# Optimization experiments

Measured on AMD Instinct MI355X. Metric: run time of the kernel, lower is better.

Reference implementation:

```python
import jax, jax.numpy as jnp
import numpy as np

B = 1024
N_ATOMS = 51
FLAT = 7 * 7 * 64  # conv output: 84->20->9->7 spatial, 64 channels


def _conv(x, w, b, s):
    # x: NCHW, w: OIHW, VALID padding, stride s
    y = jax.lax.conv_general_dilated(
        x, w, window_strides=(s, s), padding='VALID',
        dimension_numbers=('NCHW', 'OIHW', 'NCHW'))
    return y + b[None, :, None, None]


def setup_inputs() -> dict:
    key = jax.random.key(0)
    ks = jax.random.split(key, 8)

    def w(k, shape, fan_in):
        return jax.random.normal(k, shape, dtype=jnp.float32) / np.float32(np.sqrt(fan_in))

    return {
        'x': jax.random.uniform(ks[0], (B, 4, 84, 84), jnp.float32, 0.0, 256.0),
        'cw1': w(ks[1], (32, 4, 8, 8), 4 * 8 * 8), 'cb1': jnp.zeros((32,), jnp.float32),
        'cw2': w(ks[2], (64, 32, 4, 4), 32 * 4 * 4), 'cb2': jnp.zeros((64,), jnp.float32),
        'cw3': w(ks[3], (64, 64, 3, 3), 64 * 3 * 3), 'cb3': jnp.zeros((64,), jnp.float32),
        'fw1': w(ks[4], (FLAT, 256), FLAT), 'fb1': jnp.zeros((256,), jnp.float32),
        'fw2': w(ks[5], (256, N_ATOMS), 256), 'fb2': jnp.zeros((N_ATOMS,), jnp.float32),
        'z': jnp.linspace(-10.0, 10.0, N_ATOMS).astype(jnp.float32),  # support atoms
        'n_out': 6,
    }


def reference(x, cw1, cb1, cw2, cb2, cw3, cb3, fw1, fb1, fw2, fb2, z, n_out):
    x = x / 256.0
    x = jax.nn.relu(_conv(x, cw1, cb1, 4))  # [B,32,20,20]
    x = jax.nn.relu(_conv(x, cw2, cb2, 2))  # [B,64,9,9]
    x = jax.nn.relu(_conv(x, cw3, cb3, 1))  # [B,64,7,7]
    h = x.reshape(x.shape[0], -1)           # [B,3136]
    h = jax.nn.relu(h @ fw1 + fb1)          # [B,256]
    p = jax.nn.softmax(h @ fw2 + fb2, axis=1)  # [B,n_atoms]
    # Original loop writes fc_layers(x)[i] identically for every action j:
    dist = jnp.broadcast_to(p[:, None, :], (p.shape[0], n_out, p.shape[1]))
    res = jnp.einsum('bna,a->bn', dist, z)  # expected value per action
    return (dist, res)
```

## Files before the change

kernel.cpp:

```cpp
#include <hip/hip_runtime.h>
#include <hip/hip_fp16.h>

#define RL(x) __builtin_amdgcn_readfirstlane(x)

typedef _Float16 f16x8 __attribute__((ext_vector_type(8)));
typedef float    f32x16 __attribute__((ext_vector_type(16)));

__global__ __launch_bounds__(256) void wprep_k(const float* __restrict__ w1,
                                               const float* __restrict__ w2,
                                               const float* __restrict__ w3,
                                               float* __restrict__ wt1,
                                               __half* __restrict__ w2h,
                                               float* __restrict__ wt3) {
  int i = blockIdx.x * 256 + threadIdx.x;
  if (i < 8192) {
    int kx = i & 7, j = (i >> 3) & 7, g = (i >> 6) & 3;
    int ky = (i >> 8) & 7, ic = i >> 11;
    wt1[i] = w1[(g * 8 + j) * 256 + ic * 64 + ky * 8 + kx];
  }
  if (i < 32768) {
    int j = i & 7, ln = (i >> 3) & 31, kh = (i >> 8) & 1, ot = (i >> 9) & 1, ic = i >> 10;
    int k = kh * 8 + j, kx = k >> 2, ky = k & 3, oc = ot * 32 + ln;
    w2h[i] = __float2half(w2[oc * 512 + ic * 16 + ky * 4 + kx]);
  }
  if (i < 36864) {
    int o3 = i % 24, o = o3 / 3, kx = o3 - o * 3;
    int r = i / 24, ocg = r & 7, r2 = r >> 3, ky = r2 % 3, ic = r2 / 3;
    wt3[i] = w3[(ocg * 8 + o) * 576 + ic * 9 + ky * 3 + kx];
  }
}

__global__ __launch_bounds__(256, 4) void conv1_k(const float* __restrict__ x,
                                                  const float* __restrict__ wt,
                                                  const float* __restrict__ bias,
                                                  __half* __restrict__ out) {
  __shared__ float plane[7056];
  const int b    = blockIdx.x;
  const int tid  = threadIdx.x;
  const int lane = tid & 63;
  const int g    = RL(tid >> 6);

  int pv[7], ib[7];
#pragma unroll
  for (int s = 0; s < 7; ++s) {
    int p = lane + 64 * s;
    pv[s] = (p < 400);
    if (p > 399) p = 399;
    int py = p / 20, px = p - py * 20;
    ib[s] = py * 336 + px * 4;
  }

  float acc[7][8];
#pragma unroll
  for (int s = 0; s < 7; ++s)
#pragma unroll
    for (int j = 0; j < 8; ++j) acc[s][j] = 0.f;

  const float* xb = x + b * 28224;

#pragma unroll 1
  for (int ici = 0; ici < 4; ++ici) {
    const int ic = (ici + (b >> 8)) & 3;
    if (ici) __syncthreads();
    const float* xp = xb + ic * 7056;
#pragma unroll
    for (int i = 0; i < 7; ++i) {
      int idx = tid + i * 256;
      if (idx < 1764) {
        float4 v = *(const float4*)(xp + idx * 4);
        *(float4*)&plane[idx * 4] = v;
      }
    }
    __syncthreads();

#pragma unroll 1
    for (int ky = 0; ky < 8; ++ky) {
      const float* wp = wt + (ic * 8 + ky) * 256 + g * 64;
      float wr[8][8];
#pragma unroll
      for (int j = 0; j < 8; ++j) {
        float4 w0 = *(const float4*)(wp + j * 8);
        float4 w1 = *(const float4*)(wp + j * 8 + 4);
        wr[j][0]=w0.x; wr[j][1]=w0.y; wr[j][2]=w0.z; wr[j][3]=w0.w;
        wr[j][4]=w1.x; wr[j][5]=w1.y; wr[j][6]=w1.z; wr[j][7]=w1.w;
      }
      const float* rp = plane + ky * 84;
#pragma unroll
      for (int s = 0; s < 7; ++s) {
        float4 a = *(const float4*)(rp + ib[s]);
        float4 c = *(const float4*)(rp + ib[s] + 4);
        float in8[8] = {a.x, a.y, a.z, a.w, c.x, c.y, c.z, c.w};
#pragma unroll
        for (int j = 0; j < 8; ++j)
#pragma unroll
          for (int kx = 0; kx < 8; ++kx)
            acc[s][j] = fmaf(in8[kx], wr[j][kx], acc[s][j]);
      }
    }
  }

  const float inv256 = 1.0f / 256.0f;
#pragma unroll
  for (int j = 0; j < 8; ++j) {
    float bj = bias[g * 8 + j];
    __half* op = out + (b * 32 + g * 8 + j) * 400;
#pragma unroll
    for (int s = 0; s < 7; ++s) {
      if (pv[s]) {
        float v = acc[s][j] * inv256 + bj;
        op[lane + 64 * s] = __float2half(v > 0.f ? v : 0.f);
      }
    }
  }
}

__global__ __launch_bounds__(256) void t1_k(const __half* __restrict__ in,
                                            __half* __restrict__ out) {
  __shared__ __half t[64][65];
  const int kb = blockIdx.x * 64;
  const int bb = blockIdx.y * 64;
  const int lane = threadIdx.x & 63;
  const int ty   = threadIdx.x >> 6;
#pragma unroll
  for (int r = ty; r < 64; r += 4)
    t[r][lane] = in[(bb + r) * 12800 + kb + lane];
  __syncthreads();
#pragma unroll
  for (int r = ty; r < 64; r += 4)
    out[(kb + r) * 1024 + bb + lane] = t[lane][r];
}

__global__ __launch_bounds__(256, 1) void conv2_k(const __half* __restrict__ in,
                                                  const __half* __restrict__ w2h,
                                                  const float* __restrict__ bias,
                                                  __half* __restrict__ out) {
  __shared__ __align__(16) __half sh[2][9216];
  const int bid = blockIdx.x;
  const int opy = bid % 9;
  const int bt  = bid / 9;
  const int bbase = bt * 64;
  const int tid  = threadIdx.x;
  const int lane = tid & 63;
  const int wv   = RL(tid >> 6);
  const int octile = wv & 1;
  const int bsub   = wv >> 1;
  const int kh = lane >> 5;
  const int ln = lane & 31;

  const unsigned short* inu = (const unsigned short*)in;
  const unsigned short* wu  = (const unsigned short*)w2h;

  int roff[5], offA[5];
#pragma unroll
  for (int p = 0; p < 5; ++p) {
    int idx = p * 256 + tid;
    int px = idx >> 6, b = idx & 63;
    roff[p] = px * 1024 + b;
    offA[p] = b * 128 + ((((px >> 1) ^ (b & 7)) << 3) | ((px & 1) << 2));
  }
  const int base0 = (40 * opy) * 1024 + bbase;

  f32x16 acc[9];
#pragma unroll
  for (int ox = 0; ox < 9; ++ox)
#pragma unroll
    for (int r = 0; r < 16; ++r) acc[ox][r] = 0.f;

  ushort4 s0, s1, s2, s3, s4; uint2 sW;

#define C2_LOAD(icv) do {                                                     \
    const unsigned short* ibp = inu + (icv) * 409600 + base0;                 \
    s0 = make_ushort4(ibp[roff[0]], ibp[roff[0]+20480], ibp[roff[0]+40960], ibp[roff[0]+61440]); \
    s1 = make_ushort4(ibp[roff[1]], ibp[roff[1]+20480], ibp[roff[1]+40960], ibp[roff[1]+61440]); \
    s2 = make_ushort4(ibp[roff[2]], ibp[roff[2]+20480], ibp[roff[2]+40960], ibp[roff[2]+61440]); \
    s3 = make_ushort4(ibp[roff[3]], ibp[roff[3]+20480], ibp[roff[3]+40960], ibp[roff[3]+61440]); \
    s4 = make_ushort4(ibp[roff[4]], ibp[roff[4]+20480], ibp[roff[4]+40960], ibp[roff[4]+61440]); \
    sW = *(const uint2*)(wu + (icv) * 1024 + tid * 4);                        \
  } while (0)

#define C2_STORE(buf) do {                                                    \
    *(uint2*)&sh[buf][offA[0]] = make_uint2((unsigned)s0.x | ((unsigned)s0.y << 16), (unsigned)s0.z | ((unsigned)s0.w << 16)); \
    *(uint2*)&sh[buf][offA[1]] = make_uint2((unsigned)s1.x | ((unsigned)s1.y << 16), (unsigned)s1.z | ((unsigned)s1.w << 16)); \
    *(uint2*)&sh[buf][offA[2]] = make_uint2((unsigned)s2.x | ((unsigned)s2.y << 16), (unsigned)s2.z | ((unsigned)s2.w << 16)); \
    *(uint2*)&sh[buf][offA[3]] = make_uint2((unsigned)s3.x | ((unsigned)s3.y << 16), (unsigned)s3.z | ((unsigned)s3.w << 16)); \
    *(uint2*)&sh[buf][offA[4]] = make_uint2((unsigned)s4.x | ((unsigned)s4.y << 16), (unsigned)s4.z | ((unsigned)s4.w << 16)); \
    *(uint2*)&sh[buf][8192 + tid * 4] = sW;                                   \
  } while (0)

  const int offW = 8192 + octile * 512 + kh * 256 + ln * 8;
  const int bloc = bsub * 32 + ln;
  const int bx7  = bloc & 7;
  const int brow = bloc * 128;

  int cur = 0;
  C2_LOAD(0);
#pragma unroll 1
  for (int ic = 0; ic < 32; ++ic) {
    __syncthreads();
    C2_STORE(cur);
    const int icn = ic < 31 ? ic + 1 : 31;
    C2_LOAD(icn);
    __syncthreads();
    f16x8 aw = *(const f16x8*)&sh[cur][offW];
#pragma unroll
    for (int ox = 0; ox < 9; ++ox) {
      f16x8 bx = *(const f16x8*)&sh[cur][brow + (((ox + kh) ^ bx7) << 3)];
      acc[ox] = __builtin_amdgcn_mfma_f32_32x32x16_f16(aw, bx, acc[ox], 0, 0, 0);
    }
    cur ^= 1;
  }
#undef C2_LOAD
#undef C2_STORE

  float bv[16];
#pragma unroll
  for (int r = 0; r < 16; ++r)
    bv[r] = bias[octile * 32 + (r & 3) + 8 * (r >> 2) + 4 * kh];
  const int bout = bbase + bloc;
#pragma unroll
  for (int ox = 0; ox < 9; ++ox) {
#pragma unroll
    for (int r = 0; r < 16; ++r) {
      const int oc = octile * 32 + (r & 3) + 8 * (r >> 2) + 4 * kh;
      float v = acc[ox][r] + bv[r];
      out[(oc * 81 + opy * 9 + ox) * 1024 + bout] = __float2half(v > 0.f ? v : 0.f);
    }
  }
}

__global__ __launch_bounds__(128, 2) void conv3_k(const __half* __restrict__ in,
                                                  const float* __restrict__ wt,
                                                  const float* __restrict__ bias,
                                                  __half* __restrict__ out) {
  const int bid = blockIdx.x;
  const int ocg = (bid >> 3) & 15;
  const int grp = ((bid >> 7) << 3) | (bid & 7);
  const int opy = grp % 7;
  const int bg  = grp / 7;
  const int tid  = threadIdx.x;
  const int lane = tid & 63;
  const int wv   = RL(tid >> 6);

  float acc[4][7];
#pragma unroll
  for (int o = 0; o < 4; ++o)
#pragma unroll
    for (int ox = 0; ox < 7; ++ox) acc[o][ox] = 0.f;

  const __half* ib = in + bg * 64 + lane;
  const int ic0 = wv * 32;

#pragma unroll 1
  for (int ici = 0; ici < 32; ++ici) {
    const int ic = ic0 + ici;
#pragma unroll
    for (int ky = 0; ky < 3; ++ky) {
      const float* wp = wt + ((ic * 3 + ky) * 8 + (ocg >> 1)) * 24 + (ocg & 1) * 12;
      float wk[12];
#pragma unroll
      for (int q = 0; q < 12; ++q) wk[q] = wp[q];
      const __half* rp = ib + (ic * 81 + (opy + ky) * 9) * 1024;
      float iv[9];
#pragma unroll
      for (int q = 0; q < 9; ++q) iv[q] = __half2float(rp[q * 1024]);
#pragma unroll
      for (int o = 0; o < 4; ++o)
#pragma unroll
        for (int ox = 0; ox < 7; ++ox)
#pragma unroll
          for (int kx = 0; kx < 3; ++kx)
            acc[o][ox] = fmaf(iv[ox + kx], wk[o * 3 + kx], acc[o][ox]);
    }
  }

  __shared__ float red[4][7][64];
  if (wv == 1) {
#pragma unroll
    for (int o = 0; o < 4; ++o)
#pragma unroll
      for (int ox = 0; ox < 7; ++ox) red[o][ox][lane] = acc[o][ox];
  }
  __syncthreads();
  if (wv == 0) {
#pragma unroll
    for (int o = 0; o < 4; ++o) {
      const int oc = ocg * 4 + o;
      const float bj = bias[oc];
#pragma unroll
      for (int ox = 0; ox < 7; ++ox) {
        float v = acc[o][ox] + red[o][ox][lane] + bj;
        out[(oc * 49 + opy * 7 + ox) * 1024 + bg * 64 + lane] =
            __float2half(v > 0.f ? v : 0.f);
      }
    }
  }
}

__global__ __launch_bounds__(64, 2) void fc1a_k(const __half* __restrict__ a,
                                                const float* __restrict__ w,
                                                float* __restrict__ part) {
  const int bid = blockIdx.x;
  const int jg  = (bid >> 3) & 15;
  const int grp = ((bid >> 7) << 3) | (bid & 7);
  const int kc  = grp & 15;
  const int bg  = grp >> 4;
  const int lane = threadIdx.x;

  float acc[16];
#pragma unroll
  for (int j = 0; j < 16; ++j) acc[j] = 0.f;

  const __half* ap = a + kc * 196 * 1024 + bg * 64 + lane;
  const float* wp0 = w + kc * 196 * 256 + jg * 16;

#pragma unroll 4
  for (int k = 0; k < 196; ++k) {
    float av = __half2float(ap[k * 1024]);
    const float* wp = wp0 + k * 256;
#pragma unroll
    for (int j = 0; j < 16; ++j) acc[j] = fmaf(av, wp[j], acc[j]);
  }
#pragma unroll
  for (int j = 0; j < 16; ++j)
    part[(kc * 256 + jg * 16 + j) * 1024 + bg * 64 + lane] = acc[j];
}

__global__ __launch_bounds__(256) void fc1b_k(const float* __restrict__ part,
                                              const float* __restrict__ bias,
                                              float* __restrict__ h) {
  int idx = blockIdx.x * 256 + threadIdx.x;
  float s = bias[idx >> 10];
#pragma unroll
  for (int c = 0; c < 16; ++c) s += part[c * 262144 + idx];
  h[idx] = s > 0.f ? s : 0.f;
}

__global__ __launch_bounds__(256) void fc2_k(const float* __restrict__ h,
                                             const float* __restrict__ w,
                                             const float* __restrict__ bias,
                                             const float* __restrict__ z,
                                             float* __restrict__ dist,
                                             float* __restrict__ res) {
  __shared__ float wl[256 * 51];
  const int tid = threadIdx.x;
#pragma unroll
  for (int i = tid; i < 256 * 51; i += 256) wl[i] = w[i];
  __syncthreads();

  const int j   = tid & 63;
  const int b   = blockIdx.x * 4 + RL(tid >> 6);
  const int jc = j < 51 ? j : 50;
  float acc = bias[jc];
#pragma unroll 8
  for (int k = 0; k < 256; ++k)
    acc = fmaf(h[k * 1024 + b], wl[k * 51 + jc], acc);
  float logit = (j < 51) ? acc : -1e30f;
  float m = logit;
#pragma unroll
  for (int o = 32; o > 0; o >>= 1) m = fmaxf(m, __shfl_xor(m, o, 64));
  float e = (j < 51) ? __expf(logit - m) : 0.f;
  float ssum = e;
#pragma unroll
  for (int o = 32; o > 0; o >>= 1) ssum += __shfl_xor(ssum, o, 64);
  float p = e / ssum;
  float zv = (j < 51) ? z[jc] : 0.f;
  float rz = p * zv;
#pragma unroll
  for (int o = 32; o > 0; o >>= 1) rz += __shfl_xor(rz, o, 64);
  if (j < 51) {
    float* db = dist + b * 6 * 51 + j;
#pragma unroll
    for (int n = 0; n < 6; ++n) db[n * 51] = p;
  }
  if (j < 6) res[b * 6 + j] = rz;
}

extern "C" void kernel_launch(void* const* d_in, const int* in_sizes, int n_in,
                              void* d_out, int out_size, void* d_ws, size_t ws_size,
                              hipStream_t stream) {
  const float* x   = (const float*)d_in[0];
  const float* cw1 = (const float*)d_in[1];
  const float* cb1 = (const float*)d_in[2];
  const float* cw2 = (const float*)d_in[3];
  const float* cb2 = (const float*)d_in[4];
  const float* cw3 = (const float*)d_in[5];
  const float* cb3 = (const float*)d_in[6];
  const float* fw1 = (const float*)d_in[7];
  const float* fb1 = (const float*)d_in[8];
  const float* fw2 = (const float*)d_in[9];
  const float* fb2 = (const float*)d_in[10];
  const float* z   = (const float*)d_in[11];

  float* ws = (float*)d_ws;
  __half* c1h = (__half*)ws;
  __half* c1t = (__half*)(ws + 6553600);
  __half* c2t = (__half*)(ws + 13107200);
  __half* c3t = (__half*)(ws + 15761408);
  float*  pw  = ws;
  float*  h_t = ws + 4194304;

  float*  wt3n = (float*)d_out;
  float*  wt1n = (float*)d_out + 36864;
  __half* w2h  = (__half*)((float*)d_out + 45056);

  float* dist = (float*)d_out;
  float* res  = dist + 1024 * 6 * 51;

  wprep_k<<<144, 256, 0, stream>>>(cw1, cw2, cw3, wt1n, w2h, wt3n);
  conv1_k<<<1024, 256, 0, stream>>>(x, wt1n, cb1, c1h);
  t1_k<<<dim3(200, 16), 256, 0, stream>>>(c1h, c1t);
  conv2_k<<<144, 256, 0, stream>>>(c1t, w2h, cb2, c2t);
  conv3_k<<<1792, 128, 0, stream>>>(c2t, wt3n, cb3, c3t);
  fc1a_k<<<4096, 64, 0, stream>>>(c3t, fw1, pw);
  fc1b_k<<<1024, 256, 0, stream>>>(pw, fb1, h_t);
  fc2_k<<<256, 256, 0, stream>>>(h_t, fw2, fb2, z, dist, res);
}
```

Before: 418.5 us.

## Rewrite conv1 as fp16 MFMA implicit GEMM writing transposed output directly

conv1 is rewritten from scalar fp32 FMAs to 32x32x16 fp16 MFMA instructions. Each block stages a 32-image row band of the input into shared memory as fp16, with the 1/256 scaling folded in. Outputs are written straight in the [oc,p,batch] layout that conv2 expects, so the separate transpose kernel and its round trip through global memory are removed. This trades fp32 accuracy for fp16 inputs and gives up some occupancy (launch bounds drop to 2 blocks) in exchange for matrix-core throughput.

```diff
diff --git a/kernel.cpp b/kernel.cpp
--- a/kernel.cpp
+++ b/kernel.cpp
@@ -4,19 +4,19 @@
 #define RL(x) __builtin_amdgcn_readfirstlane(x)
 
 typedef _Float16 f16x8 __attribute__((ext_vector_type(8)));
+typedef _Float16 f16x4 __attribute__((ext_vector_type(4)));
 typedef float    f32x16 __attribute__((ext_vector_type(16)));
 
 __global__ __launch_bounds__(256) void wprep_k(const float* __restrict__ w1,
                                                const float* __restrict__ w2,
                                                const float* __restrict__ w3,
-                                               float* __restrict__ wt1,
+                                               __half* __restrict__ w1h,
                                                __half* __restrict__ w2h,
                                                float* __restrict__ wt3) {
   int i = blockIdx.x * 256 + threadIdx.x;
   if (i < 8192) {
-    int kx = i & 7, j = (i >> 3) & 7, g = (i >> 6) & 3;
-    int ky = (i >> 8) & 7, ic = i >> 11;
-    wt1[i] = w1[(g * 8 + j) * 256 + ic * 64 + ky * 8 + kx];
+    int kx = i & 7, oc = (i >> 3) & 31, ky = (i >> 8) & 7, ic = i >> 11;
+    w1h[i] = __float2half(w1[oc * 256 + ic * 64 + ky * 8 + kx]);
   }
   if (i < 32768) {
     int j = i & 7, ln = (i >> 3) & 31, kh = (i >> 8) & 1, ot = (i >> 9) & 1, ic = i >> 10;
@@ -30,104 +30,85 @@
   }
 }
 
-__global__ __launch_bounds__(256, 4) void conv1_k(const float* __restrict__ x,
-                                                  const float* __restrict__ wt,
+__global__ __launch_bounds__(256, 2) void conv1_k(const float* __restrict__ x,
+                                                  const __half* __restrict__ w1h,
                                                   const float* __restrict__ bias,
                                                   __half* __restrict__ out) {
-  __shared__ float plane[7056];
-  const int b    = blockIdx.x;
-  const int tid  = threadIdx.x;
+  __shared__ __align__(16) __half xs[32256];
+  const int bid = blockIdx.x;
+  const int q  = bid % 10;
+  const int bt = bid / 10;
+  const int tid = threadIdx.x;
   const int lane = tid & 63;
-  const int g    = RL(tid >> 6);
-
-  int pv[7], ib[7];
-#pragma unroll
-  for (int s = 0; s < 7; ++s) {
-    int p = lane + 64 * s;
-    pv[s] = (p < 400);
-    if (p > 399) p = 399;
-    int py = p / 20, px = p - py * 20;
-    ib[s] = py * 336 + px * 4;
-  }
-
-  float acc[7][8];
-#pragma unroll
-  for (int s = 0; s < 7; ++s)
-#pragma unroll
-    for (int j = 0; j < 8; ++j) acc[s][j] = 0.f;
-
-  const float* xb = x + b * 28224;
+  const int wv   = RL(tid >> 6);
+  const int pyl = wv >> 1;
+  const int pxq = wv & 1;
+  const int kh = lane >> 5;
+  const int ln = lane & 31;
+
+  f32x16 acc[10];
+#pragma unroll
+  for (int px = 0; px < 10; ++px)
+#pragma unroll
+    for (int r = 0; r < 16; ++r) acc[px][r] = 0.f;
+
+  const float inv = 1.0f / 256.0f;
+  const float* xb = x + bt * 32 * 28224 + q * 8 * 84;
 
 #pragma unroll 1
-  for (int ici = 0; ici < 4; ++ici) {
-    const int ic = (ici + (b >> 8)) & 3;
-    if (ici) __syncthreads();
-    const float* xp = xb + ic * 7056;
-#pragma unroll
-    for (int i = 0; i < 7; ++i) {
-      int idx = tid + i * 256;
-      if (idx < 1764) {
-        float4 v = *(const float4*)(xp + idx * 4);
-        *(float4*)&plane[idx * 4] = v;
+  for (int ic = 0; ic < 4; ++ic) {
+    if (ic) __syncthreads();
+#pragma unroll 4
+    for (int pass = 0; pass < 32; ++pass) {
+      int item = pass * 256 + tid;
+      if (item < 8064) {
+        int cg = item % 21;
+        int rb = item / 21;
+        int b = rb & 31, r = rb >> 5;
+        const float* gp = xb + b * 28224 + ic * 7056 + r * 84 + cg * 4;
+        float4 v = *(const float4*)gp;
+        __half2 h01 = __floats2half2_rn(v.x * inv, v.y * inv);
+        __half2 h23 = __floats2half2_rn(v.z * inv, v.w * inv);
+        *(uint2*)&xs[(r * 32 + b) * 84 + cg * 4] =
+            make_uint2(*(unsigned*)&h01, *(unsigned*)&h23);
       }
     }
     __syncthreads();
 
-#pragma unroll 1
-    for (int ky = 0; ky < 8; ++ky) {
-      const float* wp = wt + (ic * 8 + ky) * 256 + g * 64;
-      float wr[8][8];
-#pragma unroll
-      for (int j = 0; j < 8; ++j) {
-        float4 w0 = *(const float4*)(wp + j * 8);
-        float4 w1 = *(const float4*)(wp + j * 8 + 4);
-        wr[j][0]=w0.x; wr[j][1]=w0.y; wr[j][2]=w0.z; wr[j][3]=w0.w;
-        wr[j][4]=w1.x; wr[j][5]=w1.y; wr[j][6]=w1.z; wr[j][7]=w1.w;
+#pragma unroll
+    for (int t = 0; t < 4; ++t) {
+      f16x8 aw = *(const f16x8*)(w1h + ((ic * 8 + 2 * t + kh) * 32 + ln) * 8);
+      const __half* rp = &xs[((pyl * 4 + 2 * t + kh) * 32 + ln) * 84];
+#pragma unroll
+      for (int px = 0; px < 10; ++px) {
+        const int xg = pxq * 10 + px;
+        f16x4 lo = *(const f16x4*)(rp + 4 * xg);
+        f16x4 hi = *(const f16x4*)(rp + 4 * xg + 4);
+        f16x8 bx;
+        bx[0]=lo[0]; bx[1]=lo[1]; bx[2]=lo[2]; bx[3]=lo[3];
+        bx[4]=hi[0]; bx[5]=hi[1]; bx[6]=hi[2]; bx[7]=hi[3];
+        acc[px] = __builtin_amdgcn_mfma_f32_32x32x16_f16(aw, bx, acc[px], 0, 0, 0);
       }
-      const float* rp = plane + ky * 84;
-#pragma unroll
-      for (int s = 0; s < 7; ++s) {
-        float4 a = *(const float4*)(rp + ib[s]);
-        float4 c = *(const float4*)(rp + ib[s] + 4);
-        float in8[8] = {a.x, a.y, a.z, a.w, c.x, c.y, c.z, c.w};
-#pragma unroll
-        for (int j = 0; j < 8; ++j)
-#pragma unroll
-          for (int kx = 0; kx < 8; ++kx)
-            acc[s][j] = fmaf(in8[kx], wr[j][kx], acc[s][j]);
-      }
-    }
-  }
-
-  const float inv256 = 1.0f / 256.0f;
-#pragma unroll
-  for (int j = 0; j < 8; ++j) {
-    float bj = bias[g * 8 + j];
-    __half* op = out + (b * 32 + g * 8 + j) * 400;
-#pragma unroll
-    for (int s = 0; s < 7; ++s) {
-      if (pv[s]) {
-        float v = acc[s][j] * inv256 + bj;
-        op[lane + 64 * s] = __float2half(v > 0.f ? v : 0.f);
-      }
-    }
-  }
-}
-
-__global__ __launch_bounds__(256) void t1_k(const __half* __restrict__ in,
-                                            __half* __restrict__ out) {
-  __shared__ __half t[64][65];
-  const int kb = blockIdx.x * 64;
-  const int bb = blockIdx.y * 64;
-  const int lane = threadIdx.x & 63;
-  const int ty   = threadIdx.x >> 6;
-#pragma unroll
-  for (int r = ty; r < 64; r += 4)
-    t[r][lane] = in[(bb + r) * 12800 + kb + lane];
-  __syncthreads();
-#pragma unroll
-  for (int r = ty; r < 64; r += 4)
-    out[(kb + r) * 1024 + bb + lane] = t[lane][r];
+    }
+  }
+
+  float bv[16];
+#pragma unroll
+  for (int r = 0; r < 16; ++r)
+    bv[r] = bias[(r & 3) + 8 * (r >> 2) + 4 * kh];
+
+  const int pyg = 2 * q + pyl;
+  const int bg  = bt * 32 + ln;
+#pragma unroll
+  for (int px = 0; px < 10; ++px) {
+    const int p = pyg * 20 + pxq * 10 + px;
+#pragma unroll
+    for (int r = 0; r < 16; ++r) {
+      const int oc = (r & 3) + 8 * (r >> 2) + 4 * kh;
+      float v = acc[px][r] + bv[r];
+      out[(oc * 400 + p) * 1024 + bg] = __float2half(v > 0.f ? v : 0.f);
+    }
+  }
 }
 
 __global__ __launch_bounds__(256, 1) void conv2_k(const __half* __restrict__ in,
@@ -392,7 +373,6 @@
   const float* z   = (const float*)d_in[11];
 
   float* ws = (float*)d_ws;
-  __half* c1h = (__half*)ws;
   __half* c1t = (__half*)(ws + 6553600);
   __half* c2t = (__half*)(ws + 13107200);
   __half* c3t = (__half*)(ws + 15761408);
@@ -400,15 +380,14 @@
   float*  h_t = ws + 4194304;
 
   float*  wt3n = (float*)d_out;
-  float*  wt1n = (float*)d_out + 36864;
+  __half* w1h  = (__half*)((float*)d_out + 36864);
   __half* w2h  = (__half*)((float*)d_out + 45056);
 
   float* dist = (float*)d_out;
   float* res  = dist + 1024 * 6 * 51;
 
-  wprep_k<<<144, 256, 0, stream>>>(cw1, cw2, cw3, wt1n, w2h, wt3n);
-  conv1_k<<<1024, 256, 0, stream>>>(x, wt1n, cb1, c1h);
-  t1_k<<<dim3(200, 16), 256, 0, stream>>>(c1h, c1t);
+  wprep_k<<<144, 256, 0, stream>>>(cw1, cw2, cw3, w1h, w2h, wt3n);
+  conv1_k<<<320, 256, 0, stream>>>(x, w1h, cb1, c1t);
   conv2_k<<<144, 256, 0, stream>>>(c1t, w2h, cb2, c2t);
   conv3_k<<<1792, 128, 0, stream>>>(c2t, wt3n, cb3, c3t);
   fc1a_k<<<4096, 64, 0, stream>>>(c3t, fw1, pw);
```

Result: slower. 436.3 us (+4.2%).
